# Kernel tuning notes

Measured on AMD Instinct MI355X. Metric: run time of the kernel, lower is better.

## Reference

```python
import jax, jax.numpy as jnp
import numpy as np
import math

B, S, H, L, N, V = 4, 2048, 1024, 4, 4, 256
D = H // N
EPS = 1e-5


def setup_inputs() -> dict:
    key = jax.random.key(0)
    ks = iter(jax.random.split(key, 40))
    sc = 1.0 / math.sqrt(H)
    def w(shape, s=None):
        return jax.random.normal(next(ks), shape, dtype=jnp.float32) * (s if s is not None else sc)
    inp = {
        "input_ids": jax.random.randint(next(ks), (B, S), 0, V, dtype=jnp.int32),
        "embed": w((V, H), 0.02),
        "nm_gate_w": w((H, H)), "nm_gate_b": jnp.zeros((H,), jnp.float32),
        "nm_filter_w": w((H, H)), "nm_filter_b": jnp.zeros((H,), jnp.float32),
        "nm_ctx_w": w((2, H)), "nm_ctx_b": jnp.zeros((2,), jnp.float32),
        "q_w": w((L, H, H)), "q_b": jnp.zeros((L, H), jnp.float32),
        "k_w": w((L, H, H)), "k_b": jnp.zeros((L, H), jnp.float32),
        "v_w": w((L, H, H)), "v_b": jnp.zeros((L, H), jnp.float32),
        "gain_w": w((L, N, H)), "gain_b": jnp.zeros((L, N), jnp.float32),
        "attn_ow": w((L, H, H)), "attn_ob": jnp.zeros((L, H), jnp.float32),
        "en_w": w((L, H, H)), "en_b": jnp.zeros((L, H), jnp.float32),
        "plastic_w": w((L, H, H)),
        "fix_w": w((L, H, H)), "fix_b": jnp.zeros((L, H), jnp.float32),
        "ln_g": jnp.ones((L, H), jnp.float32), "ln_b": jnp.zeros((L, H), jnp.float32),
        "out_w": w((V, H)), "out_b": jnp.zeros((V,), jnp.float32),
    }
    return inp


def _forward(input_ids, embed, nm_gate_w, nm_gate_b, nm_filter_w, nm_filter_b,
             nm_ctx_w, nm_ctx_b, q_w, q_b, k_w, k_b, v_w, v_b, gain_w, gain_b,
             attn_ow, attn_ob, en_w, en_b, plastic_w, fix_w, fix_b, ln_g, ln_b,
             out_w, out_b):
    x = embed[input_ids]                                   # [B,S,H]
    # --- NeurotransmitterModule ---
    ctx = x.mean(axis=1)                                   # [B,H]
    nm = ctx @ nm_ctx_w.T + nm_ctx_b                       # [B,2]
    dop, nor = nm[:, :1], nm[:, 1:]                        # [B,1] each
    gate = jax.nn.sigmoid(x @ nm_gate_w.T + nm_gate_b)
    x = x * (1.0 + dop[:, None, :] * gate)
    noise = jnp.tanh(x @ nm_filter_w.T + nm_filter_b)
    x = x + nor[:, None, :] * noise
    inv_sqrt_d = 1.0 / math.sqrt(D)
    for l in range(L):
        # --- GainControlAttention ---
        q = (x @ q_w[l].T + q_b[l]).reshape(B, S, N, D).transpose(0, 2, 1, 3)
        k = (x @ k_w[l].T + k_b[l]).reshape(B, S, N, D).transpose(0, 2, 1, 3)
        v = (x @ v_w[l].T + v_b[l]).reshape(B, S, N, D).transpose(0, 2, 1, 3)
        gain = x.mean(axis=1) @ gain_w[l].T + gain_b[l]    # [B,N]
        q = q * (1.0 + gain[:, :, None, None])
        scores = jnp.einsum('bnsd,bntd->bnst', q, k) * inv_sqrt_d
        attn = jax.nn.softmax(scores, axis=-1)
        ctxv = jnp.einsum('bnst,bntd->bnsd', attn, v)
        a = ctxv.transpose(0, 2, 1, 3).reshape(B, S, H) @ attn_ow[l].T + attn_ob[l]
        x = x + a
        # --- EnergyConstrainedLayer ---
        x = jax.nn.silu(x @ en_w[l].T + en_b[l])
        # --- NeuroplasticityLayer (eval mode) ---
        x = x + (x @ fix_w[l].T + fix_b[l]) + (x @ plastic_w[l].T)
        # --- LayerNorm ---
        mu = x.mean(axis=-1, keepdims=True)
        var = jnp.mean((x - mu) ** 2, axis=-1, keepdims=True)
        x = (x - mu) * jax.lax.rsqrt(var + EPS) * ln_g[l] + ln_b[l]
    return x @ out_w.T + out_b                             # [B,S,V]


def reference(input_ids, embed, nm_gate_w, nm_gate_b, nm_filter_w, nm_filter_b,
              nm_ctx_w, nm_ctx_b, q_w, q_b, k_w, k_b, v_w, v_b, gain_w, gain_b,
              attn_ow, attn_ob, en_w, en_b, plastic_w, fix_w, fix_b, ln_g, ln_b,
              out_w, out_b):
    return _forward(input_ids, embed, nm_gate_w, nm_gate_b, nm_filter_w,
                    nm_filter_b, nm_ctx_w, nm_ctx_b, q_w, q_b, k_w, k_b, v_w,
                    v_b, gain_w, gain_b, attn_ow, attn_ob, en_w, en_b,
                    plastic_w, fix_w, fix_b, ln_g, ln_b, out_w, out_b)
```

## Files before the change

kernel.cpp:

```cpp
#include <hip/hip_runtime.h>

#define B_ 4
#define S_ 2048
#define H_ 1024
#define L_ 4
#define N_ 4
#define D_ 256
#define V_ 256
#define EPSF 1e-5f
#define WH_ ((size_t)H_ * H_)

typedef __attribute__((ext_vector_type(8))) short short8;
typedef __attribute__((ext_vector_type(4))) float f32x4;

__device__ inline float bf2f(unsigned short u) {
    union { unsigned int ui; float f; } c; c.ui = ((unsigned int)u) << 16; return c.f;
}
__device__ inline unsigned short f2bf(float f) {
    union { float f; unsigned int ui; } c; c.f = f;
    unsigned int u = c.ui;
    unsigned int r = (u + 0x7FFFu + ((u >> 16) & 1u)) >> 16;
    return (unsigned short)r;
}
__device__ inline float wave64_sum(float v) {
    for (int m = 32; m >= 1; m >>= 1) v += __shfl_xor(v, m, 64);
    return v;
}
__device__ inline void gl_lds16(const unsigned short* g, unsigned short* l) {
    __builtin_amdgcn_global_load_lds(
        (const __attribute__((address_space(1))) unsigned int*)g,
        (__attribute__((address_space(3))) unsigned int*)l, 16, 0, 0);
}

__global__ void wcvt_kernel(const float* __restrict__ W,
                            unsigned short* __restrict__ Wb, int n8) {
    int idx = blockIdx.x * 256 + threadIdx.x;
    if (idx >= n8) return;
    size_t base = (size_t)idx * 8;
    float4 a0 = *(const float4*)(W + base);
    float4 a1 = *(const float4*)(W + base + 4);
    short8 t;
    t[0] = f2bf(a0.x); t[1] = f2bf(a0.y); t[2] = f2bf(a0.z); t[3] = f2bf(a0.w);
    t[4] = f2bf(a1.x); t[5] = f2bf(a1.y); t[6] = f2bf(a1.z); t[7] = f2bf(a1.w);
    *(short8*)(Wb + base) = t;
}

__global__ void wcvt_qkv(const float* __restrict__ W,
                         unsigned short* __restrict__ Wb, int n8, int sel) {
    int idx = blockIdx.x * 256 + threadIdx.x;
    if (idx >= n8) return;
    size_t p = (size_t)idx * 8;
    size_t layer = p >> 20;
    size_t within = p & (WH_ - 1);
    size_t dst = layer * 3 * WH_ + (size_t)sel * WH_ + within;
    float4 a0 = *(const float4*)(W + p);
    float4 a1 = *(const float4*)(W + p + 4);
    short8 t;
    t[0] = f2bf(a0.x); t[1] = f2bf(a0.y); t[2] = f2bf(a0.z); t[3] = f2bf(a0.w);
    t[4] = f2bf(a1.x); t[5] = f2bf(a1.y); t[6] = f2bf(a1.z); t[7] = f2bf(a1.w);
    *(short8*)(Wb + dst) = t;
}

__global__ void wadd_kernel(const float* __restrict__ Wa, const float* __restrict__ Wb2,
                            unsigned short* __restrict__ Wo, int n8) {
    int idx = blockIdx.x * 256 + threadIdx.x;
    if (idx >= n8) return;
    size_t base = (size_t)idx * 8;
    short8 t;
#pragma unroll
    for (int e = 0; e < 8; e++) {
        size_t p = base + e;
        int pos = (int)(p & (WH_ - 1));
        float v = Wa[p] + Wb2[p] + (((pos >> 10) == (pos & (H_ - 1))) ? 1.f : 0.f);
        t[e] = f2bf(v);
    }
    *(short8*)(Wo + base) = t;
}

__global__ void gather_kernel(const int* __restrict__ ids,
                              const float* __restrict__ embed,
                              unsigned short* __restrict__ x) {
    size_t idx = (size_t)blockIdx.x * 256 + threadIdx.x;
    int bs = (int)(idx >> 10);
    int h  = (int)(idx & 1023);
    x[idx] = f2bf(embed[(size_t)ids[bs] * H_ + h]);
}

__global__ void mean_kernel(const unsigned short* __restrict__ Xin,
                            float* __restrict__ xmean) {
    int idx = blockIdx.x * 256 + threadIdx.x;
    int b = idx >> 10, h = idx & 1023;
    int s0 = blockIdx.y * 128;
    const unsigned short* p = Xin + ((size_t)b * S_ + s0) * H_ + h;
    float s = 0.f;
    for (int i = 0; i < 128; i++) s += bf2f(p[(size_t)i * H_]);
    atomicAdd(&xmean[idx], s);
}

__global__ void nm_kernel(const float* __restrict__ xmean,
                          const float* __restrict__ w,
                          const float* __restrict__ bias,
                          float* __restrict__ dopnor) {
    int wave = threadIdx.x >> 6, lane = threadIdx.x & 63;
    for (int p = wave; p < 2 * B_; p += 4) {
        int b = p >> 1, j = p & 1;
        float s = 0.f;
        for (int h = lane; h < H_; h += 64) s += xmean[b * H_ + h] * w[j * H_ + h];
        s = wave64_sum(s);
        if (lane == 0) dopnor[p] = s / (float)S_ + bias[j];
    }
}

__global__ void gain_kernel(const float* __restrict__ xmean,
                            const float* __restrict__ gw,
                            const float* __restrict__ gb,
                            float* __restrict__ qscale) {
    int wave = threadIdx.x >> 6, lane = threadIdx.x & 63;
    for (int p = wave; p < B_ * N_; p += 4) {
        int b = p >> 2, n = p & 3;
        float s = 0.f;
        for (int h = lane; h < H_; h += 64) s += xmean[b * H_ + h] * gw[n * H_ + h];
        s = wave64_sum(s);
        if (lane == 0) qscale[p] = (1.f + s / (float)S_ + gb[n]) * 0.0625f;
    }
}

__global__ __launch_bounds__(256) void gemm_bt(
    const unsigned short* __restrict__ A, const unsigned short* __restrict__ W,
    const float* __restrict__ bias, void* __restrict__ Cout,
    const unsigned short* __restrict__ X, const float* __restrict__ scal,
    int K, int Nout, int mode) {
    __shared__ unsigned short As[128 * 32];
    __shared__ unsigned short Bs[128 * 32];
    int tid = threadIdx.x;
    int wave = tid >> 6, lane = tid & 63;
    int quad = lane >> 4, l16 = lane & 15;
    int bm = blockIdx.x * 128;
    int bn = blockIdx.y * 128;
    int mw = (wave >> 1) * 64, nw = (wave & 1) * 64;

    const unsigned short* Ag = A + (size_t)(bm + wave * 16 + (lane >> 2)) * K + (lane & 3) * 8;
    const unsigned short* Wg = W + (size_t)(bn + wave * 16 + (lane >> 2)) * K + (lane & 3) * 8;
    unsigned short* ldsA = As + wave * 512;
    unsigned short* ldsB = Bs + wave * 512;
    size_t rowskip = (size_t)64 * K;

    f32x4 acc[4][4];
#pragma unroll
    for (int i = 0; i < 4; i++)
#pragma unroll
        for (int j = 0; j < 4; j++)
#pragma unroll
            for (int r = 0; r < 4; r++) acc[i][j][r] = 0.f;

    for (int kk = 0; kk < K; kk += 32) {
        __syncthreads();
        gl_lds16(Ag + kk, ldsA);
        gl_lds16(Ag + rowskip + kk, ldsA + 2048);
        gl_lds16(Wg + kk, ldsB);
        gl_lds16(Wg + rowskip + kk, ldsB + 2048);
        __syncthreads();

        short8 af[4], bfr[4];
#pragma unroll
        for (int i = 0; i < 4; i++)
            af[i] = *(const short8*)&As[(mw + i * 16 + l16) * 32 + quad * 8];
#pragma unroll
        for (int j = 0; j < 4; j++)
            bfr[j] = *(const short8*)&Bs[(nw + j * 16 + l16) * 32 + quad * 8];
#pragma unroll
        for (int i = 0; i < 4; i++)
#pragma unroll
            for (int j = 0; j < 4; j++)
                acc[i][j] = __builtin_amdgcn_mfma_f32_16x16x32_bf16(af[i], bfr[j], acc[i][j], 0, 0, 0);
    }

    if (mode == 6) {
#pragma unroll
        for (int i = 0; i < 4; i++) {
#pragma unroll
            for (int j = 0; j < 4; j++) {
                int col = bn + nw + j * 16 + l16;
                float bv = bias ? bias[col] : 0.f;
                int n = col >> 8, d = col & 255;
                int row0 = bm + mw + i * 16 + quad * 4;
                int b = row0 >> 11, s0 = row0 & 2047;
                union { unsigned short u[4]; uint2 v; } pk;
#pragma unroll
                for (int r = 0; r < 4; r++) pk.u[r] = f2bf(acc[i][j][r] + bv);
                *(uint2*)((unsigned short*)Cout +
                          ((size_t)(b * N_ + n) * D_ + d) * S_ + s0) = pk.v;
            }
        }
        return;
    }

#pragma unroll
    for (int i = 0; i < 4; i++) {
#pragma unroll
        for (int j = 0; j < 4; j++) {
            int col = bn + nw + j * 16 + l16;
            float bv = bias ? bias[col] : 0.f;
#pragma unroll
            for (int r = 0; r < 4; r++) {
                int row = bm + mw + i * 16 + quad * 4 + r;
                float v = acc[i][j][r] + bv;
                size_t off = (size_t)row * Nout + col;
                if (mode == 5) {
                    ((float*)Cout)[off] = v;
                    continue;
                }
                float outv;
                if (mode == 0) {
                    outv = v;
                } else if (mode == 1) {
                    float sig = 1.f / (1.f + __expf(-v));
                    float dop = scal[(row >> 11) * 2];
                    outv = bf2f(X[off]) * (1.f + dop * sig);
                } else if (mode == 2) {
                    float nor = scal[(row >> 11) * 2 + 1];
                    outv = bf2f(X[off]) + nor * tanhf(v);
                } else if (mode == 3) {
                    outv = v + bf2f(X[off]);
                } else {
                    outv = v * (1.f / (1.f + __expf(-v)));
                }
                ((unsigned short*)Cout)[off] = f2bf(outv);
            }
        }
    }
}

__global__ __launch_bounds__(256) void gemm_qkv(
    const unsigned short* __restrict__ A, const unsigned short* __restrict__ W,
    const float* __restrict__ qb, const float* __restrict__ kb,
    const float* __restrict__ vbb, unsigned short* __restrict__ Qo,
    unsigned short* __restrict__ Ko, unsigned short* __restrict__ Vt) {
    __shared__ unsigned short As[128 * 32];
    __shared__ unsigned short Bs[128 * 32];
    const int K = H_;
    int tid = threadIdx.x;
    int wave = tid >> 6, lane = tid & 63;
    int quad = lane >> 4, l16 = lane & 15;
    int bm = blockIdx.x * 128;
    int bn = blockIdx.y * 128;
    int mw = (wave >> 1) * 64, nw = (wave & 1) * 64;

    const unsigned short* Ag = A + (size_t)(bm + wave * 16 + (lane >> 2)) * K + (lane & 3) * 8;
    const unsigned short* Wg = W + (size_t)(bn + wave * 16 + (lane >> 2)) * K + (lane & 3) * 8;
    unsigned short* ldsA = As + wave * 512;
    unsigned short* ldsB = Bs + wave * 512;
    size_t rowskip = (size_t)64 * K;

    f32x4 acc[4][4];
#pragma unroll
    for (int i = 0; i < 4; i++)
#pragma unroll
        for (int j = 0; j < 4; j++)
#pragma unroll
            for (int r = 0; r < 4; r++) acc[i][j][r] = 0.f;

    for (int kk = 0; kk < K; kk += 32) {
        __syncthreads();
        gl_lds16(Ag + kk, ldsA);
        gl_lds16(Ag + rowskip + kk, ldsA + 2048);
        gl_lds16(Wg + kk, ldsB);
        gl_lds16(Wg + rowskip + kk, ldsB + 2048);
        __syncthreads();

        short8 af[4], bfr[4];
#pragma unroll
        for (int i = 0; i < 4; i++)
            af[i] = *(const short8*)&As[(mw + i * 16 + l16) * 32 + quad * 8];
#pragma unroll
        for (int j = 0; j < 4; j++)
            bfr[j] = *(const short8*)&Bs[(nw + j * 16 + l16) * 32 + quad * 8];
#pragma unroll
        for (int i = 0; i < 4; i++)
#pragma unroll
            for (int j = 0; j < 4; j++)
                acc[i][j] = __builtin_amdgcn_mfma_f32_16x16x32_bf16(af[i], bfr[j], acc[i][j], 0, 0, 0);
    }

    int sel = (bn + nw) >> 10;
    if (sel == 2) {
#pragma unroll
        for (int i = 0; i < 4; i++) {
#pragma unroll
            for (int j = 0; j < 4; j++) {
                int c2 = ((bn + nw) & 1023) + j * 16 + l16;
                float bv = vbb[c2];
                int n = c2 >> 8, d = c2 & 255;
                int row0 = bm + mw + i * 16 + quad * 4;
                int b = row0 >> 11, s0 = row0 & 2047;
                union { unsigned short u[4]; uint2 v; } pk;
#pragma unroll
                for (int r = 0; r < 4; r++) pk.u[r] = f2bf(acc[i][j][r] + bv);
                *(uint2*)(Vt + ((size_t)(b * N_ + n) * D_ + d) * S_ + s0) = pk.v;
            }
        }
    } else {
        unsigned short* Co = (sel == 0) ? Qo : Ko;
        const float* bias = (sel == 0) ? qb : kb;
#pragma unroll
        for (int i = 0; i < 4; i++) {
#pragma unroll
            for (int j = 0; j < 4; j++) {
                int c2 = ((bn + nw) & 1023) + j * 16 + l16;
                float bv = bias[c2];
#pragma unroll
                for (int r = 0; r < 4; r++) {
                    int row = bm + mw + i * 16 + quad * 4 + r;
                    Co[(size_t)row * H_ + c2] = f2bf(acc[i][j][r] + bv);
                }
            }
        }
    }
}

__global__ __launch_bounds__(512) void flash_attn(
    const unsigned short* __restrict__ Q, const unsigned short* __restrict__ Kg,
    const unsigned short* __restrict__ VT, const float* __restrict__ qscale,
    unsigned short* __restrict__ O) {
    __shared__ unsigned short Kb[2][64 * 256];
    __shared__ unsigned short Vb[2][256 * 64];
    __shared__ unsigned short Vones[16][72];
    __shared__ unsigned short Pl[8][16][72];

    int tid = threadIdx.x;
    int wave = tid >> 6, lane = tid & 63;
    int quad = lane >> 4, l16 = lane & 15;
    int rx = l16 & 7;
    int bnh = blockIdx.y;
    size_t base = ((size_t)(bnh >> 2) * S_) * H_ + (size_t)(bnh & 3) * D_;
    size_t vtbase = (size_t)bnh * D_ * S_;
    int qw = blockIdx.x * 128 + wave * 16;
    float scale = qscale[bnh];

    for (int c = tid; c < 16 * 72; c += 512) {
        int rr = c / 72, cc = c - rr * 72;
        Vones[rr][cc] = (rr == 0) ? (unsigned short)0x3F80 : (unsigned short)0;
    }

    int l5 = lane >> 5;
    int ks = lane & 31;
    int vrow = lane >> 3;
    int vs = lane & 7;
    int vmask = vrow & 7;

    short8 qf[8];
#pragma unroll
    for (int kk = 0; kk < 8; kk++)
        qf[kk] = *(const short8*)(Q + base +
            (size_t)(qw + l16) * H_ + kk * 32 + quad * 8);

    f32x4 o[16], osum;
#pragma unroll
    for (int c = 0; c < 16; c++)
#pragma unroll
        for (int r = 0; r < 4; r++) o[c][r] = 0.f;
#pragma unroll
    for (int r = 0; r < 4; r++) osum[r] = 0.f;
    float mrow[4];
#pragma unroll
    for (int r = 0; r < 4; r++) mrow[r] = -1e30f;

    {
#pragma unroll
        for (int k = 0; k < 4; k++) {
            int chunk = 4 * wave + k;
            int kmask = (2 * k + l5) & 7;
            int grow = 2 * chunk + l5;
            int gcol = ((ks ^ kmask)) * 8;
            gl_lds16(Kg + base + (size_t)grow * H_ + gcol, &Kb[0][chunk * 512]);
        }
#pragma unroll
        for (int k = 0; k < 4; k++) {
            int chunk = 4 * wave + k;
            int d = 8 * chunk + vrow;
            int gcol = ((vs ^ vmask)) * 8;
            gl_lds16(VT + vtbase + (size_t)d * S_ + gcol, &Vb[0][chunk * 512]);
        }
    }
    asm volatile("s_waitcnt vmcnt(0)" ::: "memory");
    __syncthreads();

    int cur = 0;
    for (int t0 = 0; t0 < S_; t0 += 64) {
        if (t0 + 64 < S_) {
            int nb = cur ^ 1;
#pragma unroll
            for (int k = 0; k < 4; k++) {
                int chunk = 4 * wave + k;
                int kmask = (2 * k + l5) & 7;
                int grow = t0 + 64 + 2 * chunk + l5;
                int gcol = ((ks ^ kmask)) * 8;
                gl_lds16(Kg + base + (size_t)grow * H_ + gcol, &Kb[nb][chunk * 512]);
            }
#pragma unroll
            for (int k = 0; k < 4; k++) {
                int chunk = 4 * wave + k;
                int d = 8 * chunk + vrow;
                int gcol = ((vs ^ vmask)) * 8;
                gl_lds16(VT + vtbase + (size_t)d * S_ + t0 + 64 + gcol, &Vb[nb][chunk * 512]);
            }
        }

        const unsigned short* Kc = Kb[cur];
        const unsigned short* Vc = Vb[cur];

        f32x4 s[4];
#pragma unroll
        for (int j = 0; j < 4; j++)
#pragma unroll
            for (int r = 0; r < 4; r++) s[j][r] = 0.f;
#pragma unroll
        for (int j = 0; j < 4; j++)
#pragma unroll
            for (int kk = 0; kk < 8; kk++) {
                short8 kf = *(const short8*)&Kc[(j * 16 + l16) * 256 +
                                                ((4 * kk + quad) ^ rx) * 8];
                s[j] = __builtin_amdgcn_mfma_f32_16x16x32_bf16(qf[kk], kf, s[j], 0, 0, 0);
            }

        float sv[4][4], mx[4];
        bool ok = true;
#pragma unroll
        for (int r = 0; r < 4; r++) {
#pragma unroll
            for (int j = 0; j < 4; j++) sv[r][j] = s[j][r] * scale;
            float m0 = fmaxf(fmaxf(sv[r][0], sv[r][1]), fmaxf(sv[r][2], sv[r][3]));
            for (int m = 8; m >= 1; m >>= 1) m0 = fmaxf(m0, __shfl_xor(m0, m, 64));
            mx[r] = m0;
            ok = ok && (m0 <= mrow[r] + 8.f);
        }
        if (__all(ok)) {
#pragma unroll
            for (int r = 0; r < 4; r++)
#pragma unroll
                for (int j = 0; j < 4; j++)
                    Pl[wave][quad * 4 + r][j * 16 + l16] =
                        f2bf(__expf(sv[r][j] - mrow[r]));
        } else {
            float alpha[4];
#pragma unroll
            for (int r = 0; r < 4; r++) {
                float mnew = fmaxf(mrow[r], mx[r]);
                alpha[r] = __expf(mrow[r] - mnew);
                mrow[r] = mnew;
#pragma unroll
                for (int j = 0; j < 4; j++)
                    Pl[wave][quad * 4 + r][j * 16 + l16] =
                        f2bf(__expf(sv[r][j] - mnew));
            }
#pragma unroll
            for (int c = 0; c < 16; c++)
#pragma unroll
                for (int r = 0; r < 4; r++) o[c][r] *= alpha[r];
#pragma unroll
            for (int r = 0; r < 4; r++) osum[r] *= alpha[r];
        }

        short8 pf0 = *(const short8*)&Pl[wave][l16][quad * 8];
        short8 pf1 = *(const short8*)&Pl[wave][l16][32 + quad * 8];
#pragma unroll
        for (int c = 0; c < 16; c++) {
            short8 vf0 = *(const short8*)&Vc[(c * 16 + l16) * 64 + (quad ^ rx) * 8];
            o[c] = __builtin_amdgcn_mfma_f32_16x16x32_bf16(pf0, vf0, o[c], 0, 0, 0);
            short8 vf1 = *(const short8*)&Vc[(c * 16 + l16) * 64 + ((4 | quad) ^ rx) * 8];
            o[c] = __builtin_amdgcn_mfma_f32_16x16x32_bf16(pf1, vf1, o[c], 0, 0, 0);
        }
        {
            short8 vs0 = *(const short8*)&Vones[l16][quad * 8];
            short8 vs1 = *(const short8*)&Vones[l16][32 + quad * 8];
            osum = __builtin_amdgcn_mfma_f32_16x16x32_bf16(pf0, vs0, osum, 0, 0, 0);
            osum = __builtin_amdgcn_mfma_f32_16x16x32_bf16(pf1, vs1, osum, 0, 0, 0);
        }

        asm volatile("s_waitcnt vmcnt(0)" ::: "memory");
        __syncthreads();
        cur ^= 1;
    }

    float invl[4];
#pragma unroll
    for (int r = 0; r < 4; r++)
        invl[r] = 1.f / __shfl(osum[r], (lane & 48), 64);
#pragma unroll
    for (int c = 0; c < 16; c++)
#pragma unroll
        for (int r = 0; r < 4; r++) {
            int row = qw + quad * 4 + r;
            int d = c * 16 + l16;
            O[base + (size_t)row * H_ + d] = f2bf(o[c][r] * invl[r]);
        }
}

__global__ __launch_bounds__(256) void ln_kernel(
    const unsigned short* __restrict__ y, const float* __restrict__ g,
    const float* __restrict__ bta, unsigned short* __restrict__ out) {
    int row = blockIdx.x;
    size_t ro = (size_t)row * H_;
    int tid = threadIdx.x;
    float t[4]; float s = 0.f, s2 = 0.f;
#pragma unroll
    for (int i = 0; i < 4; i++) {
        int h = i * 256 + tid;
        float v = bf2f(y[ro + h]);
        t[i] = v; s += v; s2 += v * v;
    }
    s = wave64_sum(s); s2 = wave64_sum(s2);
    __shared__ float sh[8];
    int wave = tid >> 6, lane = tid & 63;
    if (lane == 0) { sh[wave] = s; sh[4 + wave] = s2; }
    __syncthreads();
    s  = sh[0] + sh[1] + sh[2] + sh[3];
    s2 = sh[4] + sh[5] + sh[6] + sh[7];
    float mu = s * (1.f / H_);
    float var = s2 * (1.f / H_) - mu * mu;
    float inv = rsqrtf(var + EPSF);
#pragma unroll
    for (int i = 0; i < 4; i++) {
        int h = i * 256 + tid;
        out[ro + h] = f2bf((t[i] - mu) * inv * g[h] + bta[h]);
    }
}

extern "C" void kernel_launch(void* const* d_in, const int* in_sizes, int n_in,
                              void* d_out, int out_size, void* d_ws, size_t ws_size,
                              hipStream_t stream) {
    const int*   ids          = (const int*)d_in[0];
    const float* embed        = (const float*)d_in[1];
    const float* nm_gate_w    = (const float*)d_in[2];
    const float* nm_gate_b    = (const float*)d_in[3];
    const float* nm_filter_w  = (const float*)d_in[4];
    const float* nm_filter_b  = (const float*)d_in[5];
    const float* nm_ctx_w     = (const float*)d_in[6];
    const float* nm_ctx_b     = (const float*)d_in[7];
    const float* q_w          = (const float*)d_in[8];
    const float* q_b          = (const float*)d_in[9];
    const float* k_w          = (const float*)d_in[10];
    const float* k_b          = (const float*)d_in[11];
    const float* v_w          = (const float*)d_in[12];
    const float* v_b          = (const float*)d_in[13];
    const float* gain_w       = (const float*)d_in[14];
    const float* gain_b       = (const float*)d_in[15];
    const float* attn_ow      = (const float*)d_in[16];
    const float* attn_ob      = (const float*)d_in[17];
    const float* en_w         = (const float*)d_in[18];
    const float* en_b         = (const float*)d_in[19];
    const float* plastic_w    = (const float*)d_in[20];
    const float* fix_w        = (const float*)d_in[21];
    const float* fix_b        = (const float*)d_in[22];
    const float* ln_g         = (const float*)d_in[23];
    const float* ln_b         = (const float*)d_in[24];
    const float* out_w        = (const float*)d_in[25];
    const float* out_b        = (const float*)d_in[26];

    size_t T  = (size_t)B_ * S_ * H_;
    size_t smallBytes = ((size_t)B_ * H_ + 2 * B_ + B_ * N_ + 8) * sizeof(float);
    size_t megaElems  = 26 * WH_ + WH_ / 4;
    size_t need_base  = 4 * T * 2 + smallBytes + 2 * WH_;
    size_t need_mega  = 4 * T * 2 + smallBytes + 2 * megaElems;
    if (ws_size < need_base) return;
    bool mega = ws_size >= need_mega;

    unsigned short* X   = (unsigned short*)d_ws;
    unsigned short* Qb  = X + T;
    unsigned short* Kb  = Qb + T;
    unsigned short* Vb  = Kb + T;
    float* xmean  = (float*)(Vb + T);
    float* dopnor = xmean + (size_t)B_ * H_;
    float* qscale = dopnor + 2 * B_;
    unsigned short* Wbase = (unsigned short*)(qscale + B_ * N_ + 8);
#define WOFF(k) (Wbase + (size_t)(k) * WH_)

    const int M   = B_ * S_;
    const int W8  = (int)(WH_ / 8);
    const int WG  = (W8 + 255) / 256;
    const int W84 = (int)(4 * WH_ / 8);
    const int WG4 = (W84 + 255) / 256;
    const int W8o = V_ * H_ / 8;
    const int WGo = (W8o + 255) / 256;

    if (mega) {
        wcvt_kernel<<<WG,  256, 0, stream>>>(nm_gate_w,   WOFF(0), W8);
        wcvt_kernel<<<WG,  256, 0, stream>>>(nm_filter_w, WOFF(1), W8);
        wcvt_qkv<<<WG4, 256, 0, stream>>>(q_w, WOFF(2), W84, 0);
        wcvt_qkv<<<WG4, 256, 0, stream>>>(k_w, WOFF(2), W84, 1);
        wcvt_qkv<<<WG4, 256, 0, stream>>>(v_w, WOFF(2), W84, 2);
        wcvt_kernel<<<WG4, 256, 0, stream>>>(attn_ow, WOFF(14), W84);
        wcvt_kernel<<<WG4, 256, 0, stream>>>(en_w,    WOFF(18), W84);
        wadd_kernel<<<WG4, 256, 0, stream>>>(fix_w, plastic_w, WOFF(22), W84);
        wcvt_kernel<<<WGo, 256, 0, stream>>>(out_w, WOFF(26), W8o);
    }

    gather_kernel<<<dim3((int)(T / 256)), 256, 0, stream>>>(ids, embed, X);

    hipMemsetAsync(xmean, 0, (size_t)B_ * H_ * sizeof(float), stream);
    mean_kernel<<<dim3(B_ * H_ / 256, 16), 256, 0, stream>>>(X, xmean);
    nm_kernel<<<1, 256, 0, stream>>>(xmean, nm_ctx_w, nm_ctx_b, dopnor);

    const unsigned short* Wp;
    if (mega) Wp = WOFF(0);
    else { wcvt_kernel<<<WG, 256, 0, stream>>>(nm_gate_w, Wbase, W8); Wp = Wbase; }
    gemm_bt<<<dim3(M / 128, H_ / 128), 256, 0, stream>>>(
        X, Wp, nm_gate_b, Qb, X, dopnor, H_, H_, 1);
    if (mega) Wp = WOFF(1);
    else { wcvt_kernel<<<WG, 256, 0, stream>>>(nm_filter_w, Wbase, W8); Wp = Wbase; }
    gemm_bt<<<dim3(M / 128, H_ / 128), 256, 0, stream>>>(
        Qb, Wp, nm_filter_b, X, Qb, dopnor, H_, H_, 2);

    for (int l = 0; l < L_; l++) {
        size_t wo = (size_t)l * WH_;
        size_t bo = (size_t)l * H_;
        hipMemsetAsync(xmean, 0, (size_t)B_ * H_ * sizeof(float), stream);
        mean_kernel<<<dim3(B_ * H_ / 256, 16), 256, 0, stream>>>(X, xmean);
        gain_kernel<<<1, 256, 0, stream>>>(xmean, gain_w + (size_t)l * N_ * H_,
                                           gain_b + (size_t)l * N_, qscale);

        if (mega) {
            gemm_qkv<<<dim3(M / 128, 3 * H_ / 128), 256, 0, stream>>>(
                X, WOFF(2) + (size_t)l * 3 * WH_, q_b + bo, k_b + bo, v_b + bo,
                Qb, Kb, Vb);
        } else {
            wcvt_kernel<<<WG, 256, 0, stream>>>(q_w + wo, Wbase, W8);
            gemm_bt<<<dim3(M / 128, H_ / 128), 256, 0, stream>>>(
                X, Wbase, q_b + bo, Qb, nullptr, nullptr, H_, H_, 0);
            wcvt_kernel<<<WG, 256, 0, stream>>>(k_w + wo, Wbase, W8);
            gemm_bt<<<dim3(M / 128, H_ / 128), 256, 0, stream>>>(
                X, Wbase, k_b + bo, Kb, nullptr, nullptr, H_, H_, 0);
            wcvt_kernel<<<WG, 256, 0, stream>>>(v_w + wo, Wbase, W8);
            gemm_bt<<<dim3(M / 128, H_ / 128), 256, 0, stream>>>(
                X, Wbase, v_b + bo, Vb, nullptr, nullptr, H_, H_, 6);
        }

        flash_attn<<<dim3(S_ / 128, B_ * N_), 512, 0, stream>>>(
            Qb, Kb, Vb, qscale, Qb);

        if (mega) Wp = WOFF(14) + wo;
        else { wcvt_kernel<<<WG, 256, 0, stream>>>(attn_ow + wo, Wbase, W8); Wp = Wbase; }
        gemm_bt<<<dim3(M / 128, H_ / 128), 256, 0, stream>>>(
            Qb, Wp, attn_ob + bo, Kb, X, nullptr, H_, H_, 3);
        if (mega) Wp = WOFF(18) + wo;
        else { wcvt_kernel<<<WG, 256, 0, stream>>>(en_w + wo, Wbase, W8); Wp = Wbase; }
        gemm_bt<<<dim3(M / 128, H_ / 128), 256, 0, stream>>>(
            Kb, Wp, en_b + bo, Vb, nullptr, nullptr, H_, H_, 4);
        if (mega) Wp = WOFF(22) + wo;
        else { wadd_kernel<<<WG, 256, 0, stream>>>(fix_w + wo, plastic_w + wo, Wbase, W8); Wp = Wbase; }
        gemm_bt<<<dim3(M / 128, H_ / 128), 256, 0, stream>>>(
            Vb, Wp, fix_b + bo, Qb, nullptr, nullptr, H_, H_, 0);
        ln_kernel<<<dim3(M), 256, 0, stream>>>(Qb, ln_g + bo, ln_b + bo, X);
    }

    if (mega) Wp = WOFF(26);
    else { wcvt_kernel<<<WGo, 256, 0, stream>>>(out_w, Wbase, W8o); Wp = Wbase; }
    gemm_bt<<<dim3(M / 128, V_ / 128), 256, 0, stream>>>(
        X, Wp, out_b, (float*)d_out, nullptr, nullptr, H_, V_, 5);
#undef WOFF
}
```

Measured before the change: 1.773 ms.

## Split each key block across wave pairs so K/V fragments serve two query tiles

Result: slower. 4.399 ms (+148.1%).

```diff
diff --git a/kernel.cpp b/kernel.cpp
--- a/kernel.cpp
+++ b/kernel.cpp
@@ -324,21 +324,25 @@
     unsigned short* __restrict__ O) {
     __shared__ unsigned short Kb[2][64 * 256];
     __shared__ unsigned short Vb[2][256 * 64];
-    __shared__ unsigned short Vones[16][72];
-    __shared__ unsigned short Pl[8][16][72];
+    __shared__ unsigned short Vones[16][40];
+    __shared__ unsigned short Pl[8][32][40];
 
     int tid = threadIdx.x;
     int wave = tid >> 6, lane = tid & 63;
     int quad = lane >> 4, l16 = lane & 15;
     int rx = l16 & 7;
+    int pair = wave >> 1;
+    int khalf = wave & 1;
+    int koff = khalf * 32;
+    int kv0 = khalf * 4;
     int bnh = blockIdx.y;
     size_t base = ((size_t)(bnh >> 2) * S_) * H_ + (size_t)(bnh & 3) * D_;
     size_t vtbase = (size_t)bnh * D_ * S_;
-    int qw = blockIdx.x * 128 + wave * 16;
+    int qw = blockIdx.x * 128 + pair * 32;
     float scale = qscale[bnh];
 
-    for (int c = tid; c < 16 * 72; c += 512) {
-        int rr = c / 72, cc = c - rr * 72;
+    for (int c = tid; c < 16 * 40; c += 512) {
+        int rr = c / 40, cc = c - rr * 40;
         Vones[rr][cc] = (rr == 0) ? (unsigned short)0x3F80 : (unsigned short)0;
     }
 
@@ -348,22 +352,29 @@
     int vs = lane & 7;
     int vmask = vrow & 7;
 
-    short8 qf[8];
-#pragma unroll
-    for (int kk = 0; kk < 8; kk++)
-        qf[kk] = *(const short8*)(Q + base +
-            (size_t)(qw + l16) * H_ + kk * 32 + quad * 8);
-
-    f32x4 o[16], osum;
-#pragma unroll
-    for (int c = 0; c < 16; c++)
-#pragma unroll
-        for (int r = 0; r < 4; r++) o[c][r] = 0.f;
-#pragma unroll
-    for (int r = 0; r < 4; r++) osum[r] = 0.f;
-    float mrow[4];
-#pragma unroll
-    for (int r = 0; r < 4; r++) mrow[r] = -1e30f;
+    short8 qf[2][8];
+#pragma unroll
+    for (int rt = 0; rt < 2; rt++)
+#pragma unroll
+        for (int kk = 0; kk < 8; kk++)
+            qf[rt][kk] = *(const short8*)(Q + base +
+                (size_t)(qw + rt * 16 + l16) * H_ + kk * 32 + quad * 8);
+
+    f32x4 o[2][16], osum[2];
+#pragma unroll
+    for (int rt = 0; rt < 2; rt++) {
+#pragma unroll
+        for (int c = 0; c < 16; c++)
+#pragma unroll
+            for (int r = 0; r < 4; r++) o[rt][c][r] = 0.f;
+#pragma unroll
+        for (int r = 0; r < 4; r++) osum[rt][r] = 0.f;
+    }
+    float mrow[2][4];
+#pragma unroll
+    for (int rt = 0; rt < 2; rt++)
+#pragma unroll
+        for (int r = 0; r < 4; r++) mrow[rt][r] = -1e30f;
 
     {
 #pragma unroll
@@ -371,14 +382,14 @@
             int chunk = 4 * wave + k;
             int kmask = (2 * k + l5) & 7;
             int grow = 2 * chunk + l5;
-            int gcol = ((ks ^ kmask)) * 8;
+            int gcol = (ks ^ kmask) * 8;
             gl_lds16(Kg + base + (size_t)grow * H_ + gcol, &Kb[0][chunk * 512]);
         }
 #pragma unroll
         for (int k = 0; k < 4; k++) {
             int chunk = 4 * wave + k;
             int d = 8 * chunk + vrow;
-            int gcol = ((vs ^ vmask)) * 8;
+            int gcol = (vs ^ vmask) * 8;
             gl_lds16(VT + vtbase + (size_t)d * S_ + gcol, &Vb[0][chunk * 512]);
         }
     }
@@ -394,14 +405,14 @@
                 int chunk = 4 * wave + k;
                 int kmask = (2 * k + l5) & 7;
                 int grow = t0 + 64 + 2 * chunk + l5;
-                int gcol = ((ks ^ kmask)) * 8;
+                int gcol = (ks ^ kmask) * 8;
                 gl_lds16(Kg + base + (size_t)grow * H_ + gcol, &Kb[nb][chunk * 512]);
             }
 #pragma unroll
             for (int k = 0; k < 4; k++) {
                 int chunk = 4 * wave + k;
                 int d = 8 * chunk + vrow;
-                int gcol = ((vs ^ vmask)) * 8;
+                int gcol = (vs ^ vmask) * 8;
                 gl_lds16(VT + vtbase + (size_t)d * S_ + t0 + 64 + gcol, &Vb[nb][chunk * 512]);
             }
         }
@@ -409,72 +420,83 @@
         const unsigned short* Kc = Kb[cur];
         const unsigned short* Vc = Vb[cur];
 
-        f32x4 s[4];
-#pragma unroll
-        for (int j = 0; j < 4; j++)
-#pragma unroll
-            for (int r = 0; r < 4; r++) s[j][r] = 0.f;
-#pragma unroll
-        for (int j = 0; j < 4; j++)
+        f32x4 s[2][2];
+#pragma unroll
+        for (int rt = 0; rt < 2; rt++)
+#pragma unroll
+            for (int j = 0; j < 2; j++)
+#pragma unroll
+                for (int r = 0; r < 4; r++) s[rt][j][r] = 0.f;
+#pragma unroll
+        for (int j = 0; j < 2; j++)
 #pragma unroll
             for (int kk = 0; kk < 8; kk++) {
-                short8 kf = *(const short8*)&Kc[(j * 16 + l16) * 256 +
+                short8 kf = *(const short8*)&Kc[(koff + j * 16 + l16) * 256 +
                                                 ((4 * kk + quad) ^ rx) * 8];
-                s[j] = __builtin_amdgcn_mfma_f32_16x16x32_bf16(qf[kk], kf, s[j], 0, 0, 0);
-            }
-
-        float sv[4][4], mx[4];
+                s[0][j] = __builtin_amdgcn_mfma_f32_16x16x32_bf16(qf[0][kk], kf, s[0][j], 0, 0, 0);
+                s[1][j] = __builtin_amdgcn_mfma_f32_16x16x32_bf16(qf[1][kk], kf, s[1][j], 0, 0, 0);
+            }
+
+        float sv[2][4][2], mx[2][4];
         bool ok = true;
 #pragma unroll
-        for (int r = 0; r < 4; r++) {
-#pragma unroll
-            for (int j = 0; j < 4; j++) sv[r][j] = s[j][r] * scale;
-            float m0 = fmaxf(fmaxf(sv[r][0], sv[r][1]), fmaxf(sv[r][2], sv[r][3]));
-            for (int m = 8; m >= 1; m >>= 1) m0 = fmaxf(m0, __shfl_xor(m0, m, 64));
-            mx[r] = m0;
-            ok = ok && (m0 <= mrow[r] + 8.f);
-        }
+        for (int rt = 0; rt < 2; rt++)
+#pragma unroll
+            for (int r = 0; r < 4; r++) {
+                sv[rt][r][0] = s[rt][0][r] * scale;
+                sv[rt][r][1] = s[rt][1][r] * scale;
+                float m0 = fmaxf(sv[rt][r][0], sv[rt][r][1]);
+                for (int m = 8; m >= 1; m >>= 1) m0 = fmaxf(m0, __shfl_xor(m0, m, 64));
+                mx[rt][r] = m0;
+                ok = ok && (m0 <= mrow[rt][r] + 8.f);
+            }
         if (__all(ok)) {
 #pragma unroll
-            for (int r = 0; r < 4; r++)
-#pragma unroll
-                for (int j = 0; j < 4; j++)
-                    Pl[wave][quad * 4 + r][j * 16 + l16] =
-                        f2bf(__expf(sv[r][j] - mrow[r]));
+            for (int rt = 0; rt < 2; rt++)
+#pragma unroll
+                for (int r = 0; r < 4; r++) {
+                    Pl[wave][rt * 16 + quad * 4 + r][l16] =
+                        f2bf(__expf(sv[rt][r][0] - mrow[rt][r]));
+                    Pl[wave][rt * 16 + quad * 4 + r][16 + l16] =
+                        f2bf(__expf(sv[rt][r][1] - mrow[rt][r]));
+                }
         } else {
-            float alpha[4];
-#pragma unroll
-            for (int r = 0; r < 4; r++) {
-                float mnew = fmaxf(mrow[r], mx[r]);
-                alpha[r] = __expf(mrow[r] - mnew);
-                mrow[r] = mnew;
-#pragma unroll
-                for (int j = 0; j < 4; j++)
-                    Pl[wave][quad * 4 + r][j * 16 + l16] =
-                        f2bf(__expf(sv[r][j] - mnew));
-            }
-#pragma unroll
-            for (int c = 0; c < 16; c++)
-#pragma unroll
-                for (int r = 0; r < 4; r++) o[c][r] *= alpha[r];
-#pragma unroll
-            for (int r = 0; r < 4; r++) osum[r] *= alpha[r];
+            float alpha[2][4];
+#pragma unroll
+            for (int rt = 0; rt < 2; rt++)
+#pragma unroll
+                for (int r = 0; r < 4; r++) {
+                    float mnew = fmaxf(mrow[rt][r], mx[rt][r]);
+                    alpha[rt][r] = __expf(mrow[rt][r] - mnew);
+                    mrow[rt][r] = mnew;
+                    Pl[wave][rt * 16 + quad * 4 + r][l16] =
+                        f2bf(__expf(sv[rt][r][0] - mnew));
+                    Pl[wave][rt * 16 + quad * 4 + r][16 + l16] =
+                        f2bf(__expf(sv[rt][r][1] - mnew));
+                }
+#pragma unroll
+            for (int rt = 0; rt < 2; rt++) {
+#pragma unroll
+                for (int c = 0; c < 16; c++)
+#pragma unroll
+                    for (int r = 0; r < 4; r++) o[rt][c][r] *= alpha[rt][r];
+#pragma unroll
+                for (int r = 0; r < 4; r++) osum[rt][r] *= alpha[rt][r];
+            }
         }
 
         short8 pf0 = *(const short8*)&Pl[wave][l16][quad * 8];
-        short8 pf1 = *(const short8*)&Pl[wave][l16][32 + quad * 8];
+        short8 pf1 = *(const short8*)&Pl[wave][16 + l16][quad * 8];
 #pragma unroll
         for (int c = 0; c < 16; c++) {
-            short8 vf0 = *(const short8*)&Vc[(c * 16 + l16) * 64 + (quad ^ rx) * 8];
-            o[c] = __builtin_amdgcn_mfma_f32_16x16x32_bf16(pf0, vf0, o[c], 0, 0, 0);
-            short8 vf1 = *(const short8*)&Vc[(c * 16 + l16) * 64 + ((4 | quad) ^ rx) * 8];
-            o[c] = __builtin_amdgcn_mfma_f32_16x16x32_bf16(pf1, vf1, o[c], 0, 0, 0);
+            short8 vf = *(const short8*)&Vc[(c * 16 + l16) * 64 + ((kv0 + quad) ^ rx) * 8];
+            o[0][c] = __builtin_amdgcn_mfma_f32_16x16x32_bf16(pf0, vf, o[0][c], 0, 0, 0);
+            o[1][c] = __builtin_amdgcn_mfma_f32_16x16x32_bf16(pf1, vf, o[1][c], 0, 0, 0);
         }
         {
-            short8 vs0 = *(const short8*)&Vones[l16][quad * 8];
-            short8 vs1 = *(const short8*)&Vones[l16][32 + quad * 8];
-            osum = __builtin_amdgcn_mfma_f32_16x16x32_bf16(pf0, vs0, osum, 0, 0, 0);
-            osum = __builtin_amdgcn_mfma_f32_16x16x32_bf16(pf1, vs1, osum, 0, 0, 0);
+            short8 vsf = *(const short8*)&Vones[l16][quad * 8];
+            osum[0] = __builtin_amdgcn_mfma_f32_16x16x32_bf16(pf0, vsf, osum[0], 0, 0, 0);
+            osum[1] = __builtin_amdgcn_mfma_f32_16x16x32_bf16(pf1, vsf, osum[1], 0, 0, 0);
         }
 
         asm volatile("s_waitcnt vmcnt(0)" ::: "memory");
@@ -482,18 +504,61 @@
         cur ^= 1;
     }
 
-    float invl[4];
-#pragma unroll
-    for (int r = 0; r < 4; r++)
-        invl[r] = 1.f / __shfl(osum[r], (lane & 48), 64);
-#pragma unroll
-    for (int c = 0; c < 16; c++)
-#pragma unroll
-        for (int r = 0; r < 4; r++) {
-            int row = qw + quad * 4 + r;
-            int d = c * 16 + l16;
-            O[base + (size_t)row * H_ + d] = f2bf(o[c][r] * invl[r]);
-        }
+    float* Of = (pair < 2) ? ((float*)&Kb[0][0] + pair * 8192)
+                           : ((float*)&Vb[0][0] + (pair - 2) * 8192);
+    float* Ml = (float*)&Pl[0][0][0];
+    if (khalf) {
+#pragma unroll
+        for (int rt = 0; rt < 2; rt++)
+#pragma unroll
+            for (int c = 0; c < 16; c++) {
+                int idx = ((((rt * 16 + c) * 4 + quad) * 16) + l16) * 4;
+                *(f32x4*)&Of[idx] = o[rt][c];
+            }
+        if (l16 == 0) {
+#pragma unroll
+            for (int rt = 0; rt < 2; rt++)
+#pragma unroll
+                for (int r = 0; r < 4; r++) {
+                    int row = rt * 16 + quad * 4 + r;
+                    Ml[pair * 64 + row]      = mrow[rt][r];
+                    Ml[pair * 64 + 32 + row] = osum[rt][r];
+                }
+        }
+    }
+    __syncthreads();
+    if (!khalf) {
+        float sca[2][4], scb[2][4];
+#pragma unroll
+        for (int rt = 0; rt < 2; rt++)
+#pragma unroll
+            for (int r = 0; r < 4; r++) {
+                int row = rt * 16 + quad * 4 + r;
+                float mb = Ml[pair * 64 + row];
+                float lb = Ml[pair * 64 + 32 + row];
+                float la = __shfl(osum[rt][r], (lane & 48), 64);
+                float mm = fmaxf(mrow[rt][r], mb);
+                float ea = __expf(mrow[rt][r] - mm);
+                float eb = __expf(mb - mm);
+                float inv = 1.f / (ea * la + eb * lb);
+                sca[rt][r] = ea * inv;
+                scb[rt][r] = eb * inv;
+            }
+#pragma unroll
+        for (int rt = 0; rt < 2; rt++)
+#pragma unroll
+            for (int c = 0; c < 16; c++) {
+                int idx = ((((rt * 16 + c) * 4 + quad) * 16) + l16) * 4;
+                f32x4 ob = *(const f32x4*)&Of[idx];
+#pragma unroll
+                for (int r = 0; r < 4; r++) {
+                    int row = qw + rt * 16 + quad * 4 + r;
+                    int d = c * 16 + l16;
+                    O[base + (size_t)row * H_ + d] =
+                        f2bf(o[rt][c][r] * sca[rt][r] + ob[r] * scb[rt][r]);
+                }
+            }
+    }
 }
 
 __global__ __launch_bounds__(256) void ln_kernel(
```

## Split KV tile across wave pairs in flash attention and merge partial softmax

Applied to the files above, without the earlier changes.

Result: slower. 2.078 ms (+17.2%).

```diff
diff --git a/kernel.cpp b/kernel.cpp
--- a/kernel.cpp
+++ b/kernel.cpp
@@ -322,25 +322,23 @@
     const unsigned short* __restrict__ Q, const unsigned short* __restrict__ Kg,
     const unsigned short* __restrict__ VT, const float* __restrict__ qscale,
     unsigned short* __restrict__ O) {
-    __shared__ unsigned short Kb[2][64 * 256];
-    __shared__ unsigned short Vb[2][256 * 64];
-    __shared__ unsigned short Vones[16][72];
-    __shared__ unsigned short Pl[8][16][72];
+    __shared__ unsigned short Kt[64 * 256];
+    __shared__ unsigned short Vt[256 * 64];
+    __shared__ unsigned short Pl[8][16][40];
 
     int tid = threadIdx.x;
     int wave = tid >> 6, lane = tid & 63;
     int quad = lane >> 4, l16 = lane & 15;
     int rx = l16 & 7;
+    int pair = wave >> 1;
+    int khalf = wave & 1;
+    int koff = khalf * 32;
+    int kv0 = khalf * 4;
     int bnh = blockIdx.y;
     size_t base = ((size_t)(bnh >> 2) * S_) * H_ + (size_t)(bnh & 3) * D_;
     size_t vtbase = (size_t)bnh * D_ * S_;
-    int qw = blockIdx.x * 128 + wave * 16;
+    int qw = blockIdx.x * 64 + pair * 16;
     float scale = qscale[bnh];
-
-    for (int c = tid; c < 16 * 72; c += 512) {
-        int rr = c / 72, cc = c - rr * 72;
-        Vones[rr][cc] = (rr == 0) ? (unsigned short)0x3F80 : (unsigned short)0;
-    }
 
     int l5 = lane >> 5;
     int ks = lane & 31;
@@ -354,146 +352,143 @@
         qf[kk] = *(const short8*)(Q + base +
             (size_t)(qw + l16) * H_ + kk * 32 + quad * 8);
 
-    f32x4 o[16], osum;
+    f32x4 o[16];
 #pragma unroll
     for (int c = 0; c < 16; c++)
 #pragma unroll
         for (int r = 0; r < 4; r++) o[c][r] = 0.f;
-#pragma unroll
-    for (int r = 0; r < 4; r++) osum[r] = 0.f;
-    float mrow[4];
-#pragma unroll
-    for (int r = 0; r < 4; r++) mrow[r] = -1e30f;
-
-    {
+    float mrow[4], lsum[4];
+#pragma unroll
+    for (int r = 0; r < 4; r++) { mrow[r] = -1e30f; lsum[r] = 0.f; }
+
+    for (int t0 = 0; t0 < S_; t0 += 64) {
+        __syncthreads();
 #pragma unroll
         for (int k = 0; k < 4; k++) {
             int chunk = 4 * wave + k;
             int kmask = (2 * k + l5) & 7;
-            int grow = 2 * chunk + l5;
-            int gcol = ((ks ^ kmask)) * 8;
-            gl_lds16(Kg + base + (size_t)grow * H_ + gcol, &Kb[0][chunk * 512]);
+            int grow = t0 + 2 * chunk + l5;
+            int gcol = (ks ^ kmask) * 8;
+            gl_lds16(Kg + base + (size_t)grow * H_ + gcol, &Kt[chunk * 512]);
         }
 #pragma unroll
         for (int k = 0; k < 4; k++) {
             int chunk = 4 * wave + k;
             int d = 8 * chunk + vrow;
-            int gcol = ((vs ^ vmask)) * 8;
-            gl_lds16(VT + vtbase + (size_t)d * S_ + gcol, &Vb[0][chunk * 512]);
-        }
-    }
-    asm volatile("s_waitcnt vmcnt(0)" ::: "memory");
-    __syncthreads();
-
-    int cur = 0;
-    for (int t0 = 0; t0 < S_; t0 += 64) {
-        if (t0 + 64 < S_) {
-            int nb = cur ^ 1;
-#pragma unroll
-            for (int k = 0; k < 4; k++) {
-                int chunk = 4 * wave + k;
-                int kmask = (2 * k + l5) & 7;
-                int grow = t0 + 64 + 2 * chunk + l5;
-                int gcol = ((ks ^ kmask)) * 8;
-                gl_lds16(Kg + base + (size_t)grow * H_ + gcol, &Kb[nb][chunk * 512]);
-            }
-#pragma unroll
-            for (int k = 0; k < 4; k++) {
-                int chunk = 4 * wave + k;
-                int d = 8 * chunk + vrow;
-                int gcol = ((vs ^ vmask)) * 8;
-                gl_lds16(VT + vtbase + (size_t)d * S_ + t0 + 64 + gcol, &Vb[nb][chunk * 512]);
-            }
-        }
-
-        const unsigned short* Kc = Kb[cur];
-        const unsigned short* Vc = Vb[cur];
-
-        f32x4 s[4];
-#pragma unroll
-        for (int j = 0; j < 4; j++)
+            int gcol = (vs ^ vmask) * 8;
+            gl_lds16(VT + vtbase + (size_t)d * S_ + t0 + gcol, &Vt[chunk * 512]);
+        }
+        asm volatile("s_waitcnt vmcnt(0)" ::: "memory");
+        __syncthreads();
+
+        f32x4 s[2];
+#pragma unroll
+        for (int j = 0; j < 2; j++)
 #pragma unroll
             for (int r = 0; r < 4; r++) s[j][r] = 0.f;
 #pragma unroll
-        for (int j = 0; j < 4; j++)
+        for (int j = 0; j < 2; j++)
 #pragma unroll
             for (int kk = 0; kk < 8; kk++) {
-                short8 kf = *(const short8*)&Kc[(j * 16 + l16) * 256 +
+                short8 kf = *(const short8*)&Kt[(koff + j * 16 + l16) * 256 +
                                                 ((4 * kk + quad) ^ rx) * 8];
                 s[j] = __builtin_amdgcn_mfma_f32_16x16x32_bf16(qf[kk], kf, s[j], 0, 0, 0);
             }
 
-        float sv[4][4], mx[4];
+        float sv[4][2];
         bool ok = true;
 #pragma unroll
         for (int r = 0; r < 4; r++) {
-#pragma unroll
-            for (int j = 0; j < 4; j++) sv[r][j] = s[j][r] * scale;
-            float m0 = fmaxf(fmaxf(sv[r][0], sv[r][1]), fmaxf(sv[r][2], sv[r][3]));
+            sv[r][0] = s[0][r] * scale;
+            sv[r][1] = s[1][r] * scale;
+            float m0 = fmaxf(sv[r][0], sv[r][1]);
             for (int m = 8; m >= 1; m >>= 1) m0 = fmaxf(m0, __shfl_xor(m0, m, 64));
-            mx[r] = m0;
             ok = ok && (m0 <= mrow[r] + 8.f);
         }
         if (__all(ok)) {
 #pragma unroll
-            for (int r = 0; r < 4; r++)
-#pragma unroll
-                for (int j = 0; j < 4; j++)
-                    Pl[wave][quad * 4 + r][j * 16 + l16] =
-                        f2bf(__expf(sv[r][j] - mrow[r]));
+            for (int r = 0; r < 4; r++) {
+                float e0 = __expf(sv[r][0] - mrow[r]);
+                float e1 = __expf(sv[r][1] - mrow[r]);
+                Pl[wave][quad * 4 + r][l16]      = f2bf(e0);
+                Pl[wave][quad * 4 + r][16 + l16] = f2bf(e1);
+                float ps = e0 + e1;
+                for (int m = 8; m >= 1; m >>= 1) ps += __shfl_xor(ps, m, 64);
+                lsum[r] += ps;
+            }
         } else {
-            float alpha[4];
 #pragma unroll
             for (int r = 0; r < 4; r++) {
-                float mnew = fmaxf(mrow[r], mx[r]);
-                alpha[r] = __expf(mrow[r] - mnew);
+                float m0 = fmaxf(sv[r][0], sv[r][1]);
+                for (int m = 8; m >= 1; m >>= 1) m0 = fmaxf(m0, __shfl_xor(m0, m, 64));
+                float mnew = fmaxf(mrow[r], m0);
+                float alpha = __expf(mrow[r] - mnew);
                 mrow[r] = mnew;
-#pragma unroll
-                for (int j = 0; j < 4; j++)
-                    Pl[wave][quad * 4 + r][j * 16 + l16] =
-                        f2bf(__expf(sv[r][j] - mnew));
-            }
-#pragma unroll
-            for (int c = 0; c < 16; c++)
-#pragma unroll
-                for (int r = 0; r < 4; r++) o[c][r] *= alpha[r];
-#pragma unroll
-            for (int r = 0; r < 4; r++) osum[r] *= alpha[r];
-        }
-
-        short8 pf0 = *(const short8*)&Pl[wave][l16][quad * 8];
-        short8 pf1 = *(const short8*)&Pl[wave][l16][32 + quad * 8];
+                float e0 = __expf(sv[r][0] - mnew);
+                float e1 = __expf(sv[r][1] - mnew);
+                Pl[wave][quad * 4 + r][l16]      = f2bf(e0);
+                Pl[wave][quad * 4 + r][16 + l16] = f2bf(e1);
+                float ps = e0 + e1;
+                for (int m = 8; m >= 1; m >>= 1) ps += __shfl_xor(ps, m, 64);
+                lsum[r] = lsum[r] * alpha + ps;
+#pragma unroll
+                for (int c = 0; c < 16; c++) o[c][r] *= alpha;
+            }
+        }
+
+        short8 pf = *(const short8*)&Pl[wave][l16][quad * 8];
 #pragma unroll
         for (int c = 0; c < 16; c++) {
-            short8 vf0 = *(const short8*)&Vc[(c * 16 + l16) * 64 + (quad ^ rx) * 8];
-            o[c] = __builtin_amdgcn_mfma_f32_16x16x32_bf16(pf0, vf0, o[c], 0, 0, 0);
-            short8 vf1 = *(const short8*)&Vc[(c * 16 + l16) * 64 + ((4 | quad) ^ rx) * 8];
-            o[c] = __builtin_amdgcn_mfma_f32_16x16x32_bf16(pf1, vf1, o[c], 0, 0, 0);
-        }
-        {
-            short8 vs0 = *(const short8*)&Vones[l16][quad * 8];
-            short8 vs1 = *(const short8*)&Vones[l16][32 + quad * 8];
-            osum = __builtin_amdgcn_mfma_f32_16x16x32_bf16(pf0, vs0, osum, 0, 0, 0);
-            osum = __builtin_amdgcn_mfma_f32_16x16x32_bf16(pf1, vs1, osum, 0, 0, 0);
-        }
-
-        asm volatile("s_waitcnt vmcnt(0)" ::: "memory");
-        __syncthreads();
-        cur ^= 1;
-    }
-
-    float invl[4];
-#pragma unroll
-    for (int r = 0; r < 4; r++)
-        invl[r] = 1.f / __shfl(osum[r], (lane & 48), 64);
-#pragma unroll
-    for (int c = 0; c < 16; c++)
+            short8 vf = *(const short8*)&Vt[(c * 16 + l16) * 64 + ((kv0 + quad) ^ rx) * 8];
+            o[c] = __builtin_amdgcn_mfma_f32_16x16x32_bf16(pf, vf, o[c], 0, 0, 0);
+        }
+    }
+
+    __syncthreads();
+    float* Of = (pair < 2) ? ((float*)&Kt[0] + pair * 4096)
+                           : ((float*)&Vt[0] + (pair - 2) * 4096);
+    float* Ml = (float*)&Pl[0][0][0];
+    if (khalf) {
+#pragma unroll
+        for (int c = 0; c < 16; c++)
+            *(f32x4*)&Of[((c * 4 + quad) * 16 + l16) * 4] = o[c];
+        if (l16 == 0) {
+#pragma unroll
+            for (int r = 0; r < 4; r++) {
+                int row = quad * 4 + r;
+                Ml[pair * 32 + row]      = mrow[r];
+                Ml[pair * 32 + 16 + row] = lsum[r];
+            }
+        }
+    }
+    __syncthreads();
+    if (!khalf) {
+        float sca[4], scb[4];
 #pragma unroll
         for (int r = 0; r < 4; r++) {
-            int row = qw + quad * 4 + r;
-            int d = c * 16 + l16;
-            O[base + (size_t)row * H_ + d] = f2bf(o[c][r] * invl[r]);
-        }
+            int row = quad * 4 + r;
+            float mb = Ml[pair * 32 + row];
+            float lb = Ml[pair * 32 + 16 + row];
+            float la = lsum[r];
+            float mm = fmaxf(mrow[r], mb);
+            float ea = __expf(mrow[r] - mm);
+            float eb = __expf(mb - mm);
+            float inv = 1.f / (ea * la + eb * lb);
+            sca[r] = ea * inv;
+            scb[r] = eb * inv;
+        }
+#pragma unroll
+        for (int c = 0; c < 16; c++) {
+            f32x4 ob = *(const f32x4*)&Of[((c * 4 + quad) * 16 + l16) * 4];
+#pragma unroll
+            for (int r = 0; r < 4; r++) {
+                int row = qw + quad * 4 + r;
+                int d = c * 16 + l16;
+                O[base + (size_t)row * H_ + d] =
+                    f2bf(o[c][r] * sca[r] + ob[r] * scb[r]);
+            }
+        }
+    }
 }
 
 __global__ __launch_bounds__(256) void ln_kernel(
@@ -635,7 +630,7 @@
                 X, Wbase, v_b + bo, Vb, nullptr, nullptr, H_, H_, 6);
         }
 
-        flash_attn<<<dim3(S_ / 128, B_ * N_), 512, 0, stream>>>(
+        flash_attn<<<dim3(S_ / 64, B_ * N_), 512, 0, stream>>>(
             Qb, Kb, Vb, qscale, Qb);
 
         if (mega) Wp = WOFF(14) + wo;
```
